# Performance work log

Hardware: AMD Instinct MI355X
Metric: run time of the kernel (lower is better)

Reference implementation:

```python
import jax, jax.numpy as jnp
import numpy as np

D_MODEL = 1024
NUM_HEADS = 16
D_K = D_MODEL // NUM_HEADS
LN_EPS = 1e-5
NEG = -1e9


def setup_inputs() -> dict:
    key = jax.random.key(0)
    ks = jax.random.split(key, 12)
    B, S, D = 8, 1024, D_MODEL
    lim = 1.0 / np.sqrt(D)
    def lin(k):
        k1, k2 = jax.random.split(k)
        W = jax.random.uniform(k1, (D, D), jnp.float32, -lim, lim)
        b = jax.random.uniform(k2, (D,), jnp.float32, -lim, lim)
        return W, b
    Wq, bq = lin(ks[0])
    Wk, bk = lin(ks[1])
    Wv, bv = lin(ks[2])
    Wo, bo = lin(ks[3])
    return {
        "history_items": jax.random.normal(ks[4], (B, S, D), jnp.float32),
        "sequence_mask": jax.random.randint(ks[5], (B, S), 0, 2, jnp.int32),
        "Wq": Wq, "bq": bq, "Wk": Wk, "bk": bk,
        "Wv": Wv, "bv": bv, "Wo": Wo, "bo": bo,
        "ln_gamma": jnp.ones((D,), jnp.float32),
        "ln_beta": jnp.zeros((D,), jnp.float32),
    }


def reference(history_items, sequence_mask, Wq, bq, Wk, bk, Wv, bv, Wo, bo, ln_gamma, ln_beta):
    B, S, D = history_items.shape
    H, dk = NUM_HEADS, D_K
    # projections -> [B, H, S, dk]
    def proj(W, b):
        return (history_items @ W.T + b).reshape(B, S, H, dk).transpose(0, 2, 1, 3)
    q = proj(Wq, bq)
    k = proj(Wk, bk)
    v = proj(Wv, bv)
    # combined mask: causal [1,1,S,S] AND key-padding [B,1,1,S]
    causal = jnp.tril(jnp.ones((S, S), bool))[None, None]
    mask = jnp.logical_and(causal, (sequence_mask != 0)[:, None, None, :])
    scores = jnp.einsum('bhqd,bhkd->bhqk', q, k) / np.sqrt(dk).astype(np.float32)
    scores = jnp.where(mask, scores, NEG)
    attn = jax.nn.softmax(scores, axis=-1)
    ctx = jnp.einsum('bhqk,bhkd->bhqd', attn, v)  # [B,H,S,dk]
    concat = ctx.transpose(0, 2, 1, 3).reshape(B, S, D)
    out = concat @ Wo.T + bo
    x = out + history_items
    mu = jnp.mean(x, axis=-1, keepdims=True)
    var = jnp.mean((x - mu) ** 2, axis=-1, keepdims=True)
    return (x - mu) * jax.lax.rsqrt(var + LN_EPS) * ln_gamma + ln_beta
```

## Files before the change

### kernel.cpp

```cpp
#include <hip/hip_runtime.h>
#include <hip/hip_bf16.h>

#define B_ 8
#define S_ 1024
#define D_ 1024
#define H_ 16
#define DK_ 64
#define M_ (B_*S_)

#define QSCALE 0.1803368801111904f

typedef __attribute__((ext_vector_type(4))) float f32x4;
typedef __attribute__((ext_vector_type(8))) short bf16x8;
typedef __attribute__((ext_vector_type(4))) short s16x4;
typedef __hip_bfloat16 bf16;
typedef unsigned long long ull;

#define GLOAD_LDS16(gp, lp) __builtin_amdgcn_global_load_lds( \
    (const __attribute__((address_space(1))) void*)(gp), \
    (__attribute__((address_space(3))) void*)(lp), 16, 0, 0)

__device__ __forceinline__ bf16x8 ld8(const bf16* p){ return *(const bf16x8*)p; }

__device__ __forceinline__ short bf16bits(float f){
  bf16 h = __float2bfloat16(f);
  return __builtin_bit_cast(short, h);
}
__device__ __forceinline__ float tof(short b){
  unsigned u = ((unsigned)(unsigned short)b) << 16;
  return __builtin_bit_cast(float, u);
}

__device__ __forceinline__ bf16x8 ld8swz(const bf16* base, int row, int colb){
  int sw = colb ^ ((row & 7) << 4);
  return *(const bf16x8*)((const char*)base + row*128 + sw);
}

template<int CTRL>
__device__ __forceinline__ float dppadd(float x){
  int m = __builtin_amdgcn_update_dpp(0, __builtin_bit_cast(int,x), CTRL, 0xF, 0xF, true);
  return x + __builtin_bit_cast(float,m);
}
__device__ __forceinline__ float red16add(float x){
  x = dppadd<0xB1>(x);
  x = dppadd<0x4E>(x);
  x = dppadd<0x141>(x);
  x = dppadd<0x140>(x);
  return x;
}

__global__ __launch_bounds__(256) void cast_f32_bf16(const float* __restrict__ in,
                                                     bf16* __restrict__ out, int n){
  int i = (blockIdx.x*256 + threadIdx.x)*8;
  if (i >= n) return;
  f32x4 a = *(const f32x4*)(in+i);
  f32x4 b = *(const f32x4*)(in+i+4);
  bf16x8 o;
  #pragma unroll
  for (int c=0;c<4;c++){ o[c] = bf16bits(a[c]); o[c+4] = bf16bits(b[c]); }
  *(bf16x8*)(out+i) = o;
}

__global__ __launch_bounds__(256) void cast_w4(const float* __restrict__ w0, const float* __restrict__ w1,
                                               const float* __restrict__ w2, const float* __restrict__ w3,
                                               bf16* __restrict__ out){
  int sel = blockIdx.x >> 9;
  const float* src = (sel==0)?w0:((sel==1)?w1:((sel==2)?w2:w3));
  int i = (((blockIdx.x & 511)*256) + threadIdx.x)*8;
  f32x4 a = *(const f32x4*)(src+i);
  f32x4 b = *(const f32x4*)(src+i+4);
  bf16x8 o;
  #pragma unroll
  for (int c=0;c<4;c++){ o[c] = bf16bits(a[c]); o[c+4] = bf16bits(b[c]); }
  *(bf16x8*)(out + ((size_t)sel<<20) + i) = o;
}

__global__ __launch_bounds__(256) void vmean_kernel(const bf16* __restrict__ Vt_g,
                                                    float* __restrict__ vmean){
  int r = blockIdx.x*4 + (threadIdx.x>>6);
  int lane = threadIdx.x & 63;
  const bf16* p = Vt_g + (((size_t)r)<<10) + lane*16;
  bf16x8 a = ld8(p), c = ld8(p+8);
  float s = 0.f;
  #pragma unroll
  for (int e=0;e<8;e++) s += tof(a[e]) + tof(c[e]);
  #pragma unroll
  for (int off=1;off<64;off<<=1) s += __shfl_xor(s, off);
  if (lane==0) vmean[r] = s * (1.f/1024.f);
}

template<int MODE>
__global__ __launch_bounds__(256) void gemm128(
    const bf16* __restrict__ A,
    const bf16* __restrict__ W0, const bf16* __restrict__ W1, const bf16* __restrict__ W2,
    const float* __restrict__ b0, const float* __restrict__ b1, const float* __restrict__ b2,
    bf16* __restrict__ o0, bf16* __restrict__ o1, bf16* __restrict__ o2,
    const float* __restrict__ resid, float* __restrict__ xout)
{
  const bf16* Wsel = W0; const float* bsel = b0;
  if (MODE==0){
    int z = blockIdx.z;
    Wsel = (z==0)?W0:((z==1)?W1:W2);
    bsel = (z==0)?b0:((z==1)?b1:b2);
  }
  __shared__ bf16 smem[2*128*64];
  bf16* As = smem;
  bf16* Bs = smem + 128*64;
  const int tid = threadIdx.x, wid = tid>>6, lane = tid&63;
  const int lr = lane&15, lg = lane>>4;
  const int m0 = blockIdx.x*128, n0 = blockIdx.y*128;
  const int wr = wid>>1, wc = wid&1;
  f32x4 acc[4][4] = {};

  for (int k0=0; k0<1024; k0+=64){
    __syncthreads();
    #pragma unroll
    for (int c=0;c<4;c++){
      int ldsoff = ((c<<2)|wid)<<10;
      int off = ldsoff + (lane<<4);
      int row = off>>7;
      int colb = (off&127) ^ ((row&7)<<4);
      GLOAD_LDS16(A   + (((size_t)(m0+row))<<10) + k0 + (colb>>1), (char*)As + ldsoff);
      GLOAD_LDS16(Wsel+ (((size_t)(n0+row))<<10) + k0 + (colb>>1), (char*)Bs + ldsoff);
    }
    __syncthreads();
    bf16x8 af[4][2], bfv[4][2];
    #pragma unroll
    for (int m=0;m<4;m++){
      int row = wr*64 + m*16 + lr;
      af[m][0] = ld8swz(As, row, lg*16);
      af[m][1] = ld8swz(As, row, lg*16 + 64);
    }
    #pragma unroll
    for (int n=0;n<4;n++){
      int row = wc*64 + n*16 + lr;
      bfv[n][0] = ld8swz(Bs, row, lg*16);
      bfv[n][1] = ld8swz(Bs, row, lg*16 + 64);
    }
    #pragma unroll
    for (int m=0;m<4;m++)
      #pragma unroll
      for (int n=0;n<4;n++){
        acc[m][n] = __builtin_amdgcn_mfma_f32_16x16x32_bf16(af[m][0], bfv[n][0], acc[m][n],0,0,0);
        acc[m][n] = __builtin_amdgcn_mfma_f32_16x16x32_bf16(af[m][1], bfv[n][1], acc[m][n],0,0,0);
      }
  }

  if (MODE==0){
    if (blockIdx.z == 2){
      __syncthreads();
      #pragma unroll
      for (int n=0;n<4;n++){
        int c = wc*64 + n*16 + lr;
        float bias = bsel[n0 + c];
        #pragma unroll
        for (int m=0;m<4;m++){
          int r0 = wr*64 + m*16 + lg*4;
          s16x4 pk;
          #pragma unroll
          for (int j=0;j<4;j++) pk[j] = bf16bits(acc[m][n][j] + bias);
          *(s16x4*)((char*)smem + c*256 + ((r0*2) ^ ((c&7)<<4))) = pk;
        }
      }
      __syncthreads();
      #pragma unroll
      for (int q=0;q<8;q++){
        int idx = tid + q*256;
        int c = idx>>4, r8 = idx&15;
        bf16x8 vv = *(const bf16x8*)((char*)smem + c*256 + ((r8*16) ^ ((c&7)<<4)));
        int col = n0 + c;  int h = col>>6, dd = col&63;
        int row0 = m0 + r8*8;  int bb = row0>>10, s0 = row0&1023;
        *(bf16x8*)(o2 + ((((size_t)bb*H_ + h)*DK_ + dd)<<10) + s0) = vv;
      }
    } else {
      bf16* osel = (blockIdx.z==0) ? o0 : o1;
      const float qs = (blockIdx.z==0) ? QSCALE : 1.0f;
      #pragma unroll
      for (int n=0;n<4;n++){
        int col = n0 + wc*64 + n*16 + lr;
        float bias = bsel[col];
        int h = col>>6, dd = col&63;
        #pragma unroll
        for (int m=0;m<4;m++)
          #pragma unroll
          for (int j=0;j<4;j++){
            int row = m0 + wr*64 + m*16 + lg*4 + j;
            int bb = row>>10, s = row&1023;
            osel[((((size_t)bb*H_ + h)<<10) + s)*DK_ + dd] = __float2bfloat16((acc[m][n][j] + bias)*qs);
          }
      }
    }
  } else {
    #pragma unroll
    for (int n=0;n<4;n++){
      int col = n0 + wc*64 + n*16 + lr;
      float bias = bsel[col];
      #pragma unroll
      for (int m=0;m<4;m++)
        #pragma unroll
        for (int j=0;j<4;j++){
          int row = m0 + wr*64 + m*16 + lg*4 + j;
          size_t idx = (((size_t)row)<<10) + col;
          xout[idx] = acc[m][n][j] + bias + resid[idx];
        }
    }
  }
}

__global__ __launch_bounds__(512) void attn_kernel(
    const bf16* __restrict__ Q, const bf16* __restrict__ K, const bf16* __restrict__ Vt_g,
    const int* __restrict__ seqm, const float* __restrict__ vmean, bf16* __restrict__ ctxout)
{
  __shared__ bf16 Ks[2][64*64];
  __shared__ bf16 Vs[2][64*64];
  __shared__ bf16 Ps[8][32*72];
  __shared__ int msk[1024];
  const int tid = threadIdx.x, wid = tid>>6, lane = tid&63;
  const int lr = lane&15, lg = lane>>4;
  const int bh = blockIdx.x, xb = blockIdx.y;
  const int b = bh>>4, h = bh&15;
  const bf16* Qb  = Q    + (size_t)bh * S_ * DK_;
  const bf16* Kb  = K    + (size_t)bh * S_ * DK_;
  const bf16* Vtb = Vt_g + (size_t)bh * DK_ * S_;
  for (int i=tid;i<1024;i+=512) msk[i] = seqm[b*1024+i];

  const int g0 = 8*xb + wid;
  const int rb0 = g0*16;
  const int rb1 = (63 - g0)*16;
  bf16x8 qf[2][2];
  {
    const bf16* p0 = Qb + (size_t)(rb0+lr)*DK_ + lg*8;
    const bf16* p1 = Qb + (size_t)(rb1+lr)*DK_ + lg*8;
    qf[0][0] = ld8(p0); qf[0][1] = ld8(p0+32);
    qf[1][0] = ld8(p1); qf[1][1] = ld8(p1+32);
  }
  f32x4 cacc[2][4] = {};
  float lsum[2][4] = {};

  auto STAGE = [&](int t, int bsel){
    const int j0 = t*64;
    int off = (wid<<10) + (lane<<4);
    int row = off>>7;
    int colb = (off&127) ^ ((row&7)<<4);
    GLOAD_LDS16(Kb  + (size_t)(j0+row)*DK_ + (colb>>1), (char*)&Ks[bsel][0] + (wid<<10));
    GLOAD_LDS16(Vtb + (((size_t)row)<<10) + j0 + (colb>>1), (char*)&Vs[bsel][0] + (wid<<10));
  };

  STAGE(0, 0);
  __syncthreads();

  ull mbits = 0;
  #pragma unroll
  for (int i=0;i<64;i++) mbits |= ((ull)(msk[i*16+lr]!=0)) << i;

  const int bnt = ((1023 - 128*xb) >> 6) + 1;

  int cur = 0;
  for (int t=0; t<bnt; t++){
    if (t+1 < bnt) STAGE(t+1, cur^1);
    const int j0 = t*64;
    if (j0 <= rb1 + 15){
      const bool act0 = (j0 <= rb0 + 15);
      bf16x8 kf[4][2];
      #pragma unroll
      for (int nf=0;nf<4;nf++){
        kf[nf][0] = ld8swz(&Ks[cur][0], nf*16+lr, lg*16);
        kf[nf][1] = ld8swz(&Ks[cur][0], nf*16+lr, lg*16 + 64);
      }
      float madd[4];
      #pragma unroll
      for (int nf=0;nf<4;nf++)
        madd[nf] = ((mbits >> (t*4 + nf)) & 1ull) ? 0.f : -1.0e9f;

      #pragma unroll
      for (int mf=0;mf<2;mf++){
        if (mf==0 && !act0) continue;
        const int rbm = mf ? rb1 : rb0;
        const bool diag = (j0 + 63 > rbm);
        f32x4 sc[4] = {};
        #pragma unroll
        for (int nf=0;nf<4;nf++){
          sc[nf] = __builtin_amdgcn_mfma_f32_16x16x32_bf16(qf[mf][0], kf[nf][0], sc[nf],0,0,0);
          sc[nf] = __builtin_amdgcn_mfma_f32_16x16x32_bf16(qf[mf][1], kf[nf][1], sc[nf],0,0,0);
        }
        #pragma unroll
        for (int j=0;j<4;j++){
          int row = rbm + lg*4 + j;
          float ps = 0.f;
          #pragma unroll
          for (int nf=0;nf<4;nf++){
            float s = sc[nf][j] + madd[nf];
            if (diag){
              int col = j0 + nf*16 + lr;
              s = (col <= row) ? s : -1.0e9f;
            }
            float p = exp2f(s);
            sc[nf][j] = p;
            ps += p;
          }
          lsum[mf][j] += ps;
        }
        #pragma unroll
        for (int nf=0;nf<4;nf++)
          #pragma unroll
          for (int j=0;j<4;j++)
            Ps[wid][(mf*16+lg*4+j)*72 + nf*16+lr] = __float2bfloat16(sc[nf][j]);
      }
      bf16x8 pf[2][2];
      #pragma unroll
      for (int mf=0;mf<2;mf++){
        if (mf==0 && !act0) continue;
        const bf16* p = &Ps[wid][(mf*16+lr)*72 + lg*8];
        pf[mf][0] = *(const bf16x8*)p; pf[mf][1] = *(const bf16x8*)(p+32);
      }
      #pragma unroll
      for (int df=0;df<4;df++){
        #pragma unroll
        for (int kk=0;kk<2;kk++){
          bf16x8 vf = ld8swz(&Vs[cur][0], df*16+lr, lg*16 + kk*64);
          if (act0)
            cacc[0][df] = __builtin_amdgcn_mfma_f32_16x16x32_bf16(pf[0][kk], vf, cacc[0][df],0,0,0);
          cacc[1][df] = __builtin_amdgcn_mfma_f32_16x16x32_bf16(pf[1][kk], vf, cacc[1][df],0,0,0);
        }
      }
    }
    __syncthreads();
    cur ^= 1;
  }

  #pragma unroll
  for (int mf=0;mf<2;mf++){
    const int rbm = mf ? rb1 : rb0;
    float lt[4];
    #pragma unroll
    for (int j=0;j<4;j++) lt[j] = red16add(lsum[mf][j]);
    #pragma unroll
    for (int df=0;df<4;df++)
      #pragma unroll
      for (int j=0;j<4;j++){
        int srow = rbm + lg*4 + j;
        int dd = df*16 + lr;
        float v = cacc[mf][df][j] / lt[j];
        if (lt[j] <= 1.0e-30f) v = vmean[bh*64 + dd];
        ctxout[((size_t)b*S_ + srow)*D_ + h*DK_ + dd] = __float2bfloat16(v);
      }
  }
}

__global__ __launch_bounds__(256) void ln_kernel(const float* __restrict__ X2,
    const float* __restrict__ gamma, const float* __restrict__ beta, float* __restrict__ out)
{
  const int row = blockIdx.x, tid = threadIdx.x;
  const int lane = tid&63, wid = tid>>6;
  const f32x4* xr = (const f32x4*)(X2 + (((size_t)row)<<10));
  f32x4 v = xr[tid];
  float s  = v[0]+v[1]+v[2]+v[3];
  float s2 = v[0]*v[0]+v[1]*v[1]+v[2]*v[2]+v[3]*v[3];
  #pragma unroll
  for (int off=1;off<64;off<<=1){ s += __shfl_xor(s,off); s2 += __shfl_xor(s2,off); }
  __shared__ float red[8];
  if (lane==0){ red[wid]=s; red[wid+4]=s2; }
  __syncthreads();
  s  = red[0]+red[1]+red[2]+red[3];
  s2 = red[4]+red[5]+red[6]+red[7];
  float mu  = s*(1.f/1024.f);
  float var = s2*(1.f/1024.f) - mu*mu;
  float inv = rsqrtf(var + 1e-5f);
  f32x4 gv = ((const f32x4*)gamma)[tid], bv = ((const f32x4*)beta)[tid];
  f32x4 o;
  #pragma unroll
  for (int c=0;c<4;c++) o[c] = (v[c]-mu)*inv*gv[c] + bv[c];
  ((f32x4*)(out + (((size_t)row)<<10)))[tid] = o;
}

extern "C" void kernel_launch(void* const* d_in, const int* in_sizes, int n_in,
                              void* d_out, int out_size, void* d_ws, size_t ws_size,
                              hipStream_t stream) {
  const float* X   = (const float*)d_in[0];
  const int*   sm  = (const int*)d_in[1];
  const float* Wq  = (const float*)d_in[2];  const float* bq = (const float*)d_in[3];
  const float* Wk  = (const float*)d_in[4];  const float* bk = (const float*)d_in[5];
  const float* Wv  = (const float*)d_in[6];  const float* bv = (const float*)d_in[7];
  const float* Wo  = (const float*)d_in[8];  const float* bo = (const float*)d_in[9];
  const float* ga  = (const float*)d_in[10]; const float* be = (const float*)d_in[11];
  float* out = (float*)d_out;
  char* ws = (char*)d_ws;

  bf16* Xbf = (bf16*)(ws);
  bf16* Wqb = (bf16*)(ws + (16u<<20));
  bf16* Wkb = (bf16*)(ws + (18u<<20));
  bf16* Wvb = (bf16*)(ws + (20u<<20));
  bf16* Wob = (bf16*)(ws + (22u<<20));
  bf16* Qh  = (bf16*)(ws + (24u<<20));
  bf16* Kh  = (bf16*)(ws + (40u<<20));
  bf16* Vth = (bf16*)(ws + (56u<<20));
  bf16* Ctx = (bf16*)(ws + (72u<<20));
  float* X2 = (float*)(ws + (24u<<20));
  float* vmean = (float*)(ws + (16u<<20));

  cast_f32_bf16<<<4096,256,0,stream>>>(X,  Xbf, M_*D_);
  cast_w4<<<2048,256,0,stream>>>(Wq, Wk, Wv, Wo, Wqb);

  dim3 g1(M_/128, D_/128, 3);
  gemm128<0><<<g1,256,0,stream>>>(Xbf, Wqb,Wkb,Wvb, bq,bk,bv, Qh,Kh,Vth, nullptr, nullptr);

  vmean_kernel<<<B_*H_*DK_/4,256,0,stream>>>(Vth, vmean);

  dim3 g2(B_*H_, 4);
  attn_kernel<<<g2,512,0,stream>>>(Qh, Kh, Vth, sm, vmean, Ctx);

  dim3 g3(M_/128, D_/128, 1);
  gemm128<1><<<g3,256,0,stream>>>(Ctx, Wob,nullptr,nullptr, bo,nullptr,nullptr,
                                  nullptr,nullptr,nullptr, X, X2);

  ln_kernel<<<M_,256,0,stream>>>(X2, ga, be, out);
}
```

Baseline: 187.6 us.

## Double-buffer GEMM loads, drop vmean kernel, shrink attention LDS and tighten waits

The GEMM now double-buffers its A/B tiles in LDS. It issues the next tile's global-to-LDS loads before computing the current one, using explicit vmcnt waits and raw barriers in place of __syncthreads. The attention kernel gets the same explicit waitcnt/barrier treatment, an occupancy hint of 3, a smaller per-wave P buffer reused per row-fragment, and a byte mask. The separate vmean kernel is removed; fully masked rows now compute the V column mean inline, which is rare but slow if it happens. These aim to overlap memory latency with MFMA work and save a launch, at the cost of doubling GEMM LDS use, which may lower occupancy.

```diff
diff --git a/kernel.cpp b/kernel.cpp
--- a/kernel.cpp
+++ b/kernel.cpp
@@ -19,6 +19,9 @@
 #define GLOAD_LDS16(gp, lp) __builtin_amdgcn_global_load_lds( \
     (const __attribute__((address_space(1))) void*)(gp), \
     (__attribute__((address_space(3))) void*)(lp), 16, 0, 0)
+
+#define SBAR()   asm volatile("s_barrier" ::: "memory")
+#define VMCNT(n) asm volatile("s_waitcnt vmcnt(" #n ")" ::: "memory")
 
 __device__ __forceinline__ bf16x8 ld8(const bf16* p){ return *(const bf16x8*)p; }
 
@@ -73,20 +76,6 @@
   #pragma unroll
   for (int c=0;c<4;c++){ o[c] = bf16bits(a[c]); o[c+4] = bf16bits(b[c]); }
   *(bf16x8*)(out + ((size_t)sel<<20) + i) = o;
-}
-
-__global__ __launch_bounds__(256) void vmean_kernel(const bf16* __restrict__ Vt_g,
-                                                    float* __restrict__ vmean){
-  int r = blockIdx.x*4 + (threadIdx.x>>6);
-  int lane = threadIdx.x & 63;
-  const bf16* p = Vt_g + (((size_t)r)<<10) + lane*16;
-  bf16x8 a = ld8(p), c = ld8(p+8);
-  float s = 0.f;
-  #pragma unroll
-  for (int e=0;e<8;e++) s += tof(a[e]) + tof(c[e]);
-  #pragma unroll
-  for (int off=1;off<64;off<<=1) s += __shfl_xor(s, off);
-  if (lane==0) vmean[r] = s * (1.f/1024.f);
 }
 
 template<int MODE>
@@ -103,39 +92,46 @@
     Wsel = (z==0)?W0:((z==1)?W1:W2);
     bsel = (z==0)?b0:((z==1)?b1:b2);
   }
-  __shared__ bf16 smem[2*128*64];
-  bf16* As = smem;
-  bf16* Bs = smem + 128*64;
+  __shared__ bf16 smem[4*128*64];
   const int tid = threadIdx.x, wid = tid>>6, lane = tid&63;
   const int lr = lane&15, lg = lane>>4;
   const int m0 = blockIdx.x*128, n0 = blockIdx.y*128;
   const int wr = wid>>1, wc = wid&1;
   f32x4 acc[4][4] = {};
 
-  for (int k0=0; k0<1024; k0+=64){
-    __syncthreads();
+  auto STAGE = [&](int k0, int bsel_){
     #pragma unroll
     for (int c=0;c<4;c++){
       int ldsoff = ((c<<2)|wid)<<10;
       int off = ldsoff + (lane<<4);
       int row = off>>7;
       int colb = (off&127) ^ ((row&7)<<4);
-      GLOAD_LDS16(A   + (((size_t)(m0+row))<<10) + k0 + (colb>>1), (char*)As + ldsoff);
-      GLOAD_LDS16(Wsel+ (((size_t)(n0+row))<<10) + k0 + (colb>>1), (char*)Bs + ldsoff);
-    }
-    __syncthreads();
+      GLOAD_LDS16(A   + (((size_t)(m0+row))<<10) + k0 + (colb>>1), (char*)smem + bsel_*32768 + ldsoff);
+      GLOAD_LDS16(Wsel+ (((size_t)(n0+row))<<10) + k0 + (colb>>1), (char*)smem + bsel_*32768 + 16384 + ldsoff);
+    }
+  };
+
+  STAGE(0, 0);
+  int cur = 0;
+  for (int kt=0; kt<16; kt++){
+    if (kt < 15){ STAGE((kt+1)<<6, cur^1); VMCNT(8); }
+    else        { VMCNT(0); }
+    SBAR();
+    __builtin_amdgcn_sched_barrier(0);
+    const bf16* Asb = smem + cur*16384;
+    const bf16* Bsb = Asb + 8192;
     bf16x8 af[4][2], bfv[4][2];
     #pragma unroll
     for (int m=0;m<4;m++){
       int row = wr*64 + m*16 + lr;
-      af[m][0] = ld8swz(As, row, lg*16);
-      af[m][1] = ld8swz(As, row, lg*16 + 64);
+      af[m][0] = ld8swz(Asb, row, lg*16);
+      af[m][1] = ld8swz(Asb, row, lg*16 + 64);
     }
     #pragma unroll
     for (int n=0;n<4;n++){
       int row = wc*64 + n*16 + lr;
-      bfv[n][0] = ld8swz(Bs, row, lg*16);
-      bfv[n][1] = ld8swz(Bs, row, lg*16 + 64);
+      bfv[n][0] = ld8swz(Bsb, row, lg*16);
+      bfv[n][1] = ld8swz(Bsb, row, lg*16 + 64);
     }
     #pragma unroll
     for (int m=0;m<4;m++)
@@ -144,6 +140,9 @@
         acc[m][n] = __builtin_amdgcn_mfma_f32_16x16x32_bf16(af[m][0], bfv[n][0], acc[m][n],0,0,0);
         acc[m][n] = __builtin_amdgcn_mfma_f32_16x16x32_bf16(af[m][1], bfv[n][1], acc[m][n],0,0,0);
       }
+    __builtin_amdgcn_sched_barrier(0);
+    SBAR();
+    cur ^= 1;
   }
 
   if (MODE==0){
@@ -207,14 +206,14 @@
   }
 }
 
-__global__ __launch_bounds__(512) void attn_kernel(
+__global__ __launch_bounds__(512, 3) void attn_kernel(
     const bf16* __restrict__ Q, const bf16* __restrict__ K, const bf16* __restrict__ Vt_g,
-    const int* __restrict__ seqm, const float* __restrict__ vmean, bf16* __restrict__ ctxout)
+    const int* __restrict__ seqm, bf16* __restrict__ ctxout)
 {
   __shared__ bf16 Ks[2][64*64];
   __shared__ bf16 Vs[2][64*64];
-  __shared__ bf16 Ps[8][32*72];
-  __shared__ int msk[1024];
+  __shared__ bf16 Ps[8][16*72];
+  __shared__ unsigned char mskb[1024];
   const int tid = threadIdx.x, wid = tid>>6, lane = tid&63;
   const int lr = lane&15, lg = lane>>4;
   const int bh = blockIdx.x, xb = blockIdx.y;
@@ -222,7 +221,7 @@
   const bf16* Qb  = Q    + (size_t)bh * S_ * DK_;
   const bf16* Kb  = K    + (size_t)bh * S_ * DK_;
   const bf16* Vtb = Vt_g + (size_t)bh * DK_ * S_;
-  for (int i=tid;i<1024;i+=512) msk[i] = seqm[b*1024+i];
+  for (int i=tid;i<1024;i+=512) mskb[i] = (unsigned char)(seqm[b*1024+i]!=0);
 
   const int g0 = 8*xb + wid;
   const int rb0 = g0*16;
@@ -251,14 +250,18 @@
 
   ull mbits = 0;
   #pragma unroll
-  for (int i=0;i<64;i++) mbits |= ((ull)(msk[i*16+lr]!=0)) << i;
+  for (int i=0;i<64;i++) mbits |= ((ull)mskb[i*16+lr]) << i;
 
   const int bnt = ((1023 - 128*xb) >> 6) + 1;
 
   int cur = 0;
   for (int t=0; t<bnt; t++){
-    if (t+1 < bnt) STAGE(t+1, cur^1);
+    if (t+1 < bnt){ STAGE(t+1, cur^1); VMCNT(2); }
+    else          { VMCNT(0); }
+    SBAR();
+    __builtin_amdgcn_sched_barrier(0);
     const int j0 = t*64;
+    bf16x8 pf[2][2];
     if (j0 <= rb1 + 15){
       const bool act0 = (j0 <= rb0 + 15);
       bf16x8 kf[4][2];
@@ -304,14 +307,10 @@
         for (int nf=0;nf<4;nf++)
           #pragma unroll
           for (int j=0;j<4;j++)
-            Ps[wid][(mf*16+lg*4+j)*72 + nf*16+lr] = __float2bfloat16(sc[nf][j]);
-      }
-      bf16x8 pf[2][2];
-      #pragma unroll
-      for (int mf=0;mf<2;mf++){
-        if (mf==0 && !act0) continue;
-        const bf16* p = &Ps[wid][(mf*16+lr)*72 + lg*8];
-        pf[mf][0] = *(const bf16x8*)p; pf[mf][1] = *(const bf16x8*)(p+32);
+            Ps[wid][(lg*4+j)*72 + nf*16+lr] = __float2bfloat16(sc[nf][j]);
+        const bf16* pp = &Ps[wid][lr*72 + lg*8];
+        pf[mf][0] = *(const bf16x8*)pp;
+        pf[mf][1] = *(const bf16x8*)(pp+32);
       }
       #pragma unroll
       for (int df=0;df<4;df++){
@@ -324,7 +323,8 @@
         }
       }
     }
-    __syncthreads();
+    __builtin_amdgcn_sched_barrier(0);
+    SBAR();
     cur ^= 1;
   }
 
@@ -341,7 +341,16 @@
         int srow = rbm + lg*4 + j;
         int dd = df*16 + lr;
         float v = cacc[mf][df][j] / lt[j];
-        if (lt[j] <= 1.0e-30f) v = vmean[bh*64 + dd];
+        if (lt[j] <= 0.f){
+          float s = 0.f;
+          const bf16* vr = Vtb + (((size_t)dd)<<10);
+          for (int ss=0; ss<1024; ss+=8){
+            bf16x8 a8 = ld8(vr+ss);
+            #pragma unroll
+            for (int e=0;e<8;e++) s += tof(a8[e]);
+          }
+          v = s * (1.f/1024.f);
+        }
         ctxout[((size_t)b*S_ + srow)*D_ + h*DK_ + dd] = __float2bfloat16(v);
       }
   }
@@ -396,7 +405,6 @@
   bf16* Vth = (bf16*)(ws + (56u<<20));
   bf16* Ctx = (bf16*)(ws + (72u<<20));
   float* X2 = (float*)(ws + (24u<<20));
-  float* vmean = (float*)(ws + (16u<<20));
 
   cast_f32_bf16<<<4096,256,0,stream>>>(X,  Xbf, M_*D_);
   cast_w4<<<2048,256,0,stream>>>(Wq, Wk, Wv, Wo, Wqb);
@@ -404,10 +412,8 @@
   dim3 g1(M_/128, D_/128, 3);
   gemm128<0><<<g1,256,0,stream>>>(Xbf, Wqb,Wkb,Wvb, bq,bk,bv, Qh,Kh,Vth, nullptr, nullptr);
 
-  vmean_kernel<<<B_*H_*DK_/4,256,0,stream>>>(Vth, vmean);
-
   dim3 g2(B_*H_, 4);
-  attn_kernel<<<g2,512,0,stream>>>(Qh, Kh, Vth, sm, vmean, Ctx);
+  attn_kernel<<<g2,512,0,stream>>>(Qh, Kh, Vth, sm, Ctx);
 
   dim3 g3(M_/128, D_/128, 1);
   gemm128<1><<<g3,256,0,stream>>>(Ctx, Wob,nullptr,nullptr, bo,nullptr,nullptr,
```

Result: slower. 298.1 us (+59.0%).
